# Kernel optimization log

Measured on AMD Instinct MI355X. Metric: run time of the kernel, lower is better.

The kernel has to match this reference:

```python
import jax, jax.numpy as jnp
import numpy as np

B, N, DIM, H, HD = 8, 1024, 512, 8, 64
INNER = H * HD  # 512
KS = 5


def setup_inputs() -> dict:
    key = jax.random.key(0)
    ks = jax.random.split(key, 9)
    r = lambda k, shape, s=1.0: jax.random.normal(k, shape, dtype=jnp.float32) * s
    return {
        "x_1": r(ks[0], (B, N, DIM)),
        "x_2": r(ks[1], (B, N, DIM)),
        "Wqkv1": r(ks[2], (DIM, 4 * INNER), 0.02),
        "Wqkv2": r(ks[3], (DIM, 4 * INNER), 0.02),
        "Wout1": r(ks[4], (INNER, DIM), 0.02),
        "bout1": jnp.zeros((DIM,), jnp.float32),
        "Wout2": r(ks[5], (INNER, DIM), 0.02),
        "bout2": jnp.zeros((DIM,), jnp.float32),
        "conv_w": r(ks[6], (N, 1, KS), 0.1),   # depthwise Conv1d weight [out=N, in/groups=1, k]
        "conv_b": r(ks[7], (N,), 0.02),
    }


def _split_heads(t):
    # 'b n (h d) -> b h n d'
    b, n, _ = t.shape
    return t.reshape(b, n, H, HD).transpose(0, 2, 1, 3)


def _merge_heads(t):
    # 'b h n d -> b n (h d)'
    b, h, n, d = t.shape
    return t.transpose(0, 2, 1, 3).reshape(b, n, h * d)


def reference(x_1, x_2, Wqkv1, Wqkv2, Wout1, bout1, Wout2, bout2, conv_w, conv_b):
    scale = HD ** (-0.5)
    q1, k1, v1, s1 = map(_split_heads, jnp.split(x_1 @ Wqkv1, 4, axis=-1))
    q2, k2, v2, s2 = map(_split_heads, jnp.split(x_2 @ Wqkv2, 4, axis=-1))

    dots1 = jnp.einsum('bhid,bhjd->bhij', q1, k1) * scale
    dots2 = jnp.einsum('bhid,bhjd->bhij', q2, k2) * scale

    MS = _merge_heads(s1 + s2)  # [b, n, inner_dim]
    # depthwise conv over the feature axis, channels = tokens (n), kernel 5 pad 2
    A = jax.lax.conv_general_dilated(
        MS, conv_w, window_strides=(1,), padding=((KS // 2, KS // 2),),
        dimension_numbers=('NCH', 'OIH', 'NCH'), feature_group_count=N,
    ) + conv_b[None, :, None]
    MSg = jax.nn.sigmoid(A) * MS
    MSh = _split_heads(MSg)
    dots3 = jnp.einsum('bhid,bhjd->bhij', MSh, MSh) * scale

    a1 = jax.nn.softmax(dots1, axis=-1)
    a2 = jax.nn.softmax(dots2, axis=-1)
    a3 = jax.nn.softmax(dots3, axis=-1)

    t1 = jnp.einsum('bhij,bhjd->bhid', a3, v1) + v1
    t1 = jnp.einsum('bhij,bhjd->bhid', a1, t1)
    t2 = jnp.einsum('bhij,bhjd->bhid', a3, v2) + v2
    t2 = jnp.einsum('bhij,bhjd->bhid', a2, t2)

    out1 = _merge_heads(t1) @ Wout1 + bout1
    out2 = _merge_heads(t2) @ Wout2 + bout2
    return (out1, out2)
```

## Files before the change

### kernel.cpp

```cpp
#include <hip/hip_runtime.h>
#include <hip/hip_bf16.h>

#define B_     8
#define N_     1024
#define DIM_   512
#define H_     8
#define HD_    64
#define INNER_ 512
#define QKVC   2048
#define M_     8192

typedef __attribute__((ext_vector_type(8))) short short8;
typedef __attribute__((ext_vector_type(4))) float f32x4;
#define MFMA_BF16 __builtin_amdgcn_mfma_f32_16x16x32_bf16

__device__ __forceinline__ unsigned short f2b(float x) {
    __hip_bfloat16 h = __float2bfloat16(x);
    unsigned short u; __builtin_memcpy(&u, &h, 2); return u;
}
__device__ __forceinline__ unsigned int packsplit(float x) {
    unsigned int hb = f2b(x);
    float fh = __uint_as_float(hb << 16);
    unsigned int lb = f2b(x - fh);
    return (hb << 16) | lb;
}
__device__ __forceinline__ void split8(const float* v, short8& h, short8& l) {
#pragma unroll
    for (int i = 0; i < 8; i++) {
        unsigned int hb = f2b(v[i]);
        float fh = __uint_as_float(hb << 16);
        h[i] = (short)hb; l[i] = (short)f2b(v[i] - fh);
    }
}
__device__ __forceinline__ void split2x2(float a, float b, unsigned int& h, unsigned int& l) {
    unsigned int ha = f2b(a), hb = f2b(b);
    float fa = __uint_as_float(ha << 16), fb = __uint_as_float(hb << 16);
    h = ha | (hb << 16);
    l = (unsigned int)f2b(a - fa) | ((unsigned int)f2b(b - fb) << 16);
}

__device__ __forceinline__ void gll16(const unsigned short* g, unsigned short* l) {
    __builtin_amdgcn_global_load_lds(
        (const __attribute__((address_space(1))) void*)g,
        (__attribute__((address_space(3))) void*)l, 16, 0, 0);
}


__global__ __launch_bounds__(256)
void pack_a_tiled(const float* __restrict__ in, unsigned short* __restrict__ out)
{
    size_t i = ((size_t)blockIdx.x * 256 + threadIdx.x) * 4;
    float4 v = *(const float4*)(in + i);
    const size_t R = i >> 9;
    const int k  = (int)(i & 511);
    const int kt = k >> 5, kk = k & 31;
    const int r  = (int)(R & 127);
    const size_t rt = R >> 7;
    unsigned short* tile = out + (((rt << 4) + kt) << 13) + r * 64;
    unsigned int h01, l01, h23, l23;
    split2x2(v.x, v.y, h01, l01);
    split2x2(v.z, v.w, h23, l23);
    uint2 hv; hv.x = h01; hv.y = h23;
    uint2 lv; lv.x = l01; lv.y = l23;
    const int s7 = r & 7;
    *(uint2*)&tile[(((kk >> 3)     ^ s7) << 3) + (kk & 7)] = hv;
    *(uint2*)&tile[((((kk >> 3)+4) ^ s7) << 3) + (kk & 7)] = lv;
}

__global__ __launch_bounds__(256)
void pack_w_tiled(const float* __restrict__ W, unsigned short* __restrict__ out, int N)
{
    const int n  = blockIdx.x * 256 + threadIdx.x;
    const int k0 = blockIdx.y * 4;
    float f0 = W[(size_t)(k0 + 0) * N + n];
    float f1 = W[(size_t)(k0 + 1) * N + n];
    float f2 = W[(size_t)(k0 + 2) * N + n];
    float f3 = W[(size_t)(k0 + 3) * N + n];
    const int r  = n & 127;
    const size_t rt = n >> 7;
    const int kt = k0 >> 5, kk = k0 & 31;
    unsigned short* tile = out + (((rt << 4) + kt) << 13) + r * 64;
    unsigned int h01, l01, h23, l23;
    split2x2(f0, f1, h01, l01);
    split2x2(f2, f3, h23, l23);
    uint2 hv; hv.x = h01; hv.y = h23;
    uint2 lv; lv.x = l01; lv.y = l23;
    const int s7 = r & 7;
    *(uint2*)&tile[(((kk >> 3)     ^ s7) << 3) + (kk & 7)] = hv;
    *(uint2*)&tile[((((kk >> 3)+4) ^ s7) << 3) + (kk & 7)] = lv;
}

__global__ __launch_bounds__(256)
void pack_wt(const float* __restrict__ W, unsigned int* __restrict__ Wt, int N)
{
    const int n = blockIdx.x * 256 + threadIdx.x;
    const int k0 = blockIdx.y * 4;
    uint4 p;
    p.x = packsplit(W[(size_t)(k0 + 0) * N + n]);
    p.y = packsplit(W[(size_t)(k0 + 1) * N + n]);
    p.z = packsplit(W[(size_t)(k0 + 2) * N + n]);
    p.w = packsplit(W[(size_t)(k0 + 3) * N + n]);
    *(uint4*)&Wt[(size_t)n * 512 + k0] = p;
}

template<bool BIAS, bool PACKK>
__global__ __launch_bounds__(256)
void gemm_gll(const unsigned short* __restrict__ At, const unsigned short* __restrict__ Bt,
              const float* __restrict__ bias, float* __restrict__ Cp,
              int M, int N)
{
    __shared__ __align__(16) unsigned short sA[128 * 64];
    __shared__ __align__(16) unsigned short sB[128 * 64];

    const int t    = threadIdx.x;
    const int lane = t & 63;
    const int w    = t >> 6;
    const int n16  = lane & 15, quad = lane >> 4;
    const int wm   = w >> 1, wn = w & 1;
    const int m0 = blockIdx.y * 128, n0 = blockIdx.x * 128;

    f32x4 acc[4][4];
#pragma unroll
    for (int mt = 0; mt < 4; mt++)
#pragma unroll
        for (int nt = 0; nt < 4; nt++) acc[mt][nt] = (f32x4){0.f, 0.f, 0.f, 0.f};

    const unsigned short* Ag = At + ((size_t)blockIdx.y << 4) * 8192 + (w * 64 + lane) * 8;
    const unsigned short* Bg = Bt + ((size_t)blockIdx.x << 4) * 8192 + (w * 64 + lane) * 8;
    unsigned short* sAw = &sA[w * 512];
    unsigned short* sBw = &sB[w * 512];

    for (int kt = 0; kt < 16; kt++) {
        __syncthreads();
        const size_t ko = (size_t)kt * 8192;
#pragma unroll
        for (int i = 0; i < 4; i++) {
            gll16(Ag + ko + i * 2048, sAw + i * 2048);
            gll16(Bg + ko + i * 2048, sBw + i * 2048);
        }
        __syncthreads();

        short8 Ah[4], Al[4];
#pragma unroll
        for (int mt = 0; mt < 4; mt++) {
            const int row = 64 * wm + 16 * mt + n16;
            const int base = row * 64;
            const int s7 = row & 7;
            Ah[mt] = *(const short8*)&sA[base + (((quad    ) ^ s7) << 3)];
            Al[mt] = *(const short8*)&sA[base + (((quad + 4) ^ s7) << 3)];
        }
#pragma unroll
        for (int nt = 0; nt < 4; nt++) {
            const int row = 64 * wn + 16 * nt + n16;
            const int base = row * 64;
            const int s7 = row & 7;
            short8 Bh = *(const short8*)&sB[base + (((quad    ) ^ s7) << 3)];
            short8 Bl = *(const short8*)&sB[base + (((quad + 4) ^ s7) << 3)];
#pragma unroll
            for (int mt = 0; mt < 4; mt++) {
                acc[mt][nt] = MFMA_BF16(Ah[mt], Bh, acc[mt][nt], 0, 0, 0);
                acc[mt][nt] = MFMA_BF16(Al[mt], Bh, acc[mt][nt], 0, 0, 0);
                acc[mt][nt] = MFMA_BF16(Ah[mt], Bl, acc[mt][nt], 0, 0, 0);
            }
        }
    }

    const bool packout = PACKK && ((n0 >> 9) == 1);
    float bv[4];
#pragma unroll
    for (int nt = 0; nt < 4; nt++)
        bv[nt] = BIAS ? bias[n0 + 64 * wn + 16 * nt + n16] : 0.f;
#pragma unroll
    for (int mt = 0; mt < 4; mt++) {
        const int rbase = m0 + 64 * wm + 16 * mt + 4 * quad;
#pragma unroll
        for (int r = 0; r < 4; r++) {
#pragma unroll
            for (int nt = 0; nt < 4; nt++) {
                const int col = n0 + 64 * wn + 16 * nt + n16;
                const int row = rbase + r;
                const float v = acc[mt][nt][r] + bv[nt];
                if (packout) {
                    const int dg = col & 511;
                    unsigned int hb = f2b(v);
                    float fh = __uint_as_float(hb << 16);
                    unsigned short* kim = (unsigned short*)Cp + (size_t)row * (2 * N);
                    kim[1024 + dg] = (unsigned short)hb;
                    kim[1536 + dg] = f2b(v - fh);
                } else {
                    Cp[(size_t)row * N + col] = v;
                }
            }
        }
    }
}

template<bool BIAS>
__global__ __launch_bounds__(256)
void gemm_mfma(const unsigned int* __restrict__ Ap, const unsigned int* __restrict__ Btp,
               const float* __restrict__ bias, float* __restrict__ Cp,
               int M, int N)
{
    const int K = 512;
    __shared__ __align__(16) unsigned short sA[128 * 64];
    __shared__ __align__(16) unsigned short sB[128 * 64];

    const int t    = threadIdx.x;
    const int lane = t & 63;
    const int w    = t >> 6;
    const int n16  = lane & 15, quad = lane >> 4;
    const int wm   = w >> 1, wn = w & 1;
    const int m0 = blockIdx.y * 128, n0 = blockIdx.x * 128;

    f32x4 acc[4][4];
#pragma unroll
    for (int mt = 0; mt < 4; mt++)
#pragma unroll
        for (int nt = 0; nt < 4; nt++) acc[mt][nt] = (f32x4){0.f, 0.f, 0.f, 0.f};

    const int srow = t >> 1;
    const int kb   = (t & 1) * 16;
    const unsigned int* ag = Ap  + (size_t)(m0 + srow) * K + kb;
    const unsigned int* bg = Btp + (size_t)(n0 + srow) * K + kb;
    const int s7s = srow & 7;
    unsigned short* swA = &sA[srow * 64];
    unsigned short* swB = &sB[srow * 64];

    for (int k0 = 0; k0 < K; k0 += 32) {
        __syncthreads();
#pragma unroll
        for (int i = 0; i < 4; i++) {
            const int kk = kb + i * 4;
            const int ch = kk >> 3;
            const int ho = kk & 4;
            const int c_hi = ((ch    ) ^ s7s) << 3;
            const int c_lo = ((ch + 4) ^ s7s) << 3;
            uint4 va = *(const uint4*)(ag + k0 + i * 4);
            uint4 vb = *(const uint4*)(bg + k0 + i * 4);
            uint2 ha, la, hb, lb;
            ha.x = (va.y & 0xFFFF0000u) | (va.x >> 16);
            ha.y = (va.w & 0xFFFF0000u) | (va.z >> 16);
            la.x = (va.y << 16) | (va.x & 0xFFFFu);
            la.y = (va.w << 16) | (va.z & 0xFFFFu);
            hb.x = (vb.y & 0xFFFF0000u) | (vb.x >> 16);
            hb.y = (vb.w & 0xFFFF0000u) | (vb.z >> 16);
            lb.x = (vb.y << 16) | (vb.x & 0xFFFFu);
            lb.y = (vb.w << 16) | (vb.z & 0xFFFFu);
            *(uint2*)&swA[c_hi + ho] = ha;
            *(uint2*)&swA[c_lo + ho] = la;
            *(uint2*)&swB[c_hi + ho] = hb;
            *(uint2*)&swB[c_lo + ho] = lb;
        }
        __syncthreads();

        short8 Ah[4], Al[4];
#pragma unroll
        for (int mt = 0; mt < 4; mt++) {
            const int row = 64 * wm + 16 * mt + n16;
            const int base = row * 64;
            const int s7 = row & 7;
            Ah[mt] = *(const short8*)&sA[base + (((quad    ) ^ s7) << 3)];
            Al[mt] = *(const short8*)&sA[base + (((quad + 4) ^ s7) << 3)];
        }
#pragma unroll
        for (int nt = 0; nt < 4; nt++) {
            const int row = 64 * wn + 16 * nt + n16;
            const int base = row * 64;
            const int s7 = row & 7;
            short8 Bh = *(const short8*)&sB[base + (((quad    ) ^ s7) << 3)];
            short8 Bl = *(const short8*)&sB[base + (((quad + 4) ^ s7) << 3)];
#pragma unroll
            for (int mt = 0; mt < 4; mt++) {
                acc[mt][nt] = MFMA_BF16(Ah[mt], Bh, acc[mt][nt], 0, 0, 0);
                acc[mt][nt] = MFMA_BF16(Al[mt], Bh, acc[mt][nt], 0, 0, 0);
                acc[mt][nt] = MFMA_BF16(Ah[mt], Bl, acc[mt][nt], 0, 0, 0);
            }
        }
    }

    float bv[4];
#pragma unroll
    for (int nt = 0; nt < 4; nt++)
        bv[nt] = BIAS ? bias[n0 + 64 * wn + 16 * nt + n16] : 0.f;
#pragma unroll
    for (int mt = 0; mt < 4; mt++) {
        const int rbase = m0 + 64 * wm + 16 * mt + 4 * quad;
#pragma unroll
        for (int r = 0; r < 4; r++) {
#pragma unroll
            for (int nt = 0; nt < 4; nt++) {
                const int col = n0 + 64 * wn + 16 * nt + n16;
                Cp[(size_t)(rbase + r) * N + col] = acc[mt][nt][r] + bv[nt];
            }
        }
    }
}

__global__ __launch_bounds__(128)
void convgate_kernel(const float* __restrict__ qkv1, const float* __restrict__ qkv2,
                     const float* __restrict__ convw,
                     const float* __restrict__ convb,
                     float* __restrict__ MSg, unsigned short* __restrict__ Kimg)
{
    __shared__ float ms[INNER_];
    const int blk = blockIdx.x;
    const int n = blk & (N_ - 1);
    const int b = blk >> 10;
    const int t = threadIdx.x;

    const float4* q1 = (const float4*)(qkv1 + (size_t)blk * QKVC + 3 * INNER_);
    const float4* q2 = (const float4*)(qkv2 + (size_t)blk * QKVC + 3 * INNER_);
    float4 v1 = q1[t], v2 = q2[t];
    float4 s;
    s.x = v1.x + v2.x; s.y = v1.y + v2.y; s.z = v1.z + v2.z; s.w = v1.w + v2.w;
    *(float4*)&ms[t * 4] = s;
    __syncthreads();

    float w[5];
#pragma unroll
    for (int k = 0; k < 5; k++) w[k] = convw[n * 5 + k];
    const float cb = convb[n];

    float out[4];
#pragma unroll
    for (int ff = 0; ff < 4; ff++) {
        int f = t * 4 + ff;
        float A = cb;
#pragma unroll
        for (int k = 0; k < 5; k++) {
            int idx = f + k - 2;
            if (idx >= 0 && idx < INNER_) A += ms[idx] * w[k];
        }
        float sg = 1.f / (1.f + __expf(-A));
        out[ff] = ms[f] * sg;
    }
    *(float4*)&MSg[(size_t)blk * INNER_ + t * 4] = make_float4(out[0], out[1], out[2], out[3]);

    const int h  = t >> 4;
    const int d0 = (4 * t) & 63;
    unsigned short hs[4], ls[4];
#pragma unroll
    for (int e = 0; e < 4; e++) {
        unsigned int hb = f2b(out[e]);
        float fh = __uint_as_float(hb << 16);
        hs[e] = (unsigned short)hb;
        ls[e] = f2b(out[e] - fh);
    }
    unsigned short* kim = Kimg + ((size_t)(b * 8 + h) * 1024 + n) * 128 + d0;
    uint2 hv; hv.x = (unsigned int)hs[0] | ((unsigned int)hs[1] << 16);
              hv.y = (unsigned int)hs[2] | ((unsigned int)hs[3] << 16);
    uint2 lv; lv.x = (unsigned int)ls[0] | ((unsigned int)ls[1] << 16);
              lv.y = (unsigned int)ls[2] | ((unsigned int)ls[3] << 16);
    *(uint2*)kim        = hv;
    *(uint2*)(kim + 64) = lv;
}

template<int NV, bool RESID, bool PACKO, bool IMGO, bool VIMG, int NPROB>
__global__ __launch_bounds__(512, 2)
void mattn_kernel(const float* __restrict__ Q0, const float* __restrict__ Q1,
                  const unsigned short* __restrict__ K0, const unsigned short* __restrict__ K1,
                  const float* __restrict__ VA0, const float* __restrict__ VA1,
                  const float* __restrict__ VB0, const float* __restrict__ VB1,
                  float* __restrict__ OA0, float* __restrict__ OA1,
                  float* __restrict__ OB0, float* __restrict__ OB1,
                  long long q_sb, long long q_sh, int q_sr,
                  long long k_sb, long long k_sh, int k_rs, int k_po,
                  long long v_sb, long long v_sh, int v_sr,
                  long long o_sb, long long o_sh, int o_sr)
{
    __shared__ __align__(16) unsigned short sK[64 * 128];
    __shared__ __align__(16) unsigned short sV0[64 * 64];
    __shared__ __align__(16) unsigned short sV1[(NV == 2) ? 64 * 64 : 8];
    __shared__ __align__(16) unsigned short sP[128 * 64];

    const int t    = threadIdx.x;
    const int w    = t >> 6;
    const int lane = t & 63;
    const int n16  = lane & 15;
    const int quad = lane >> 4;

    const int bid = blockIdx.x;
    const int c   = bid & 7;
    const int r1  = bid >> 3;
    const int qt  = r1 & 7;
    const int r2  = r1 >> 3;
    const int g   = r2 & 7;
    const int p   = (NPROB == 2) ? (r2 >> 3) : 0;
    const int bh  = 8 * g + c;
    const int b = bh >> 3, h = bh & 7;
    const int i0 = qt * 128;

    const float* Qb          = (NPROB == 2 && p) ? Q1 : Q0;
    const unsigned short* Kb = (NPROB == 2 && p) ? K1 : K0;
    const float* VAb         = (NPROB == 2 && p) ? VA1 : VA0;
    float* OAb               = (NPROB == 2 && p) ? OA1 : OA0;

    const float* Qg          = Qb + (size_t)b * q_sb + (size_t)h * q_sh;
    const unsigned short* Kg = Kb + (size_t)b * k_sb + (size_t)h * k_sh;

    const float* V0g = nullptr;
    const float* V1g = nullptr;
    const unsigned short* Vus = nullptr;
    if constexpr (VIMG) {
        Vus = (const unsigned short*)VAb + (size_t)b * v_sb + (size_t)h * v_sh;
    } else {
        V0g = VAb + (size_t)b * v_sb + (size_t)h * v_sh;
        if constexpr (NV == 2)
            V1g = VB0 + (size_t)b * v_sb + (size_t)h * v_sh;
    }

    float* O0g = nullptr; float* O1g = nullptr;
    unsigned short* img0 = nullptr; unsigned short* img1 = nullptr;
    if constexpr (IMGO) {
        img0 = (unsigned short*)OAb + (size_t)b * o_sb + (size_t)h * o_sh;
        if constexpr (NV == 2)
            img1 = (unsigned short*)OB0 + (size_t)b * o_sb + (size_t)h * o_sh;
    } else {
        O0g = OAb + (size_t)b * o_sb + (size_t)h * o_sh;
        if constexpr (NV == 2)
            O1g = OB0 + (size_t)b * o_sb + (size_t)h * o_sh;
    }

    const float SC2 = 0.1803368801f;
    short8 Qh[2], Ql[2];
#pragma unroll
    for (int s = 0; s < 2; s++) {
        const float* qp = Qg + (size_t)(i0 + 16 * w + n16) * q_sr + 32 * s + 8 * quad;
        float qv[8];
        float4 q0 = *(const float4*)qp;
        float4 q1 = *(const float4*)(qp + 4);
        qv[0]=q0.x*SC2; qv[1]=q0.y*SC2; qv[2]=q0.z*SC2; qv[3]=q0.w*SC2;
        qv[4]=q1.x*SC2; qv[5]=q1.y*SC2; qv[6]=q1.z*SC2; qv[7]=q1.w*SC2;
        split8(qv, Qh[s], Ql[s]);
    }

    float m_ = -1e30f, l_ = 0.f;
    f32x4 O0a[4], O1a[(NV == 2) ? 4 : 1];
#pragma unroll
    for (int nt = 0; nt < 4; nt++) O0a[nt] = (f32x4){0.f,0.f,0.f,0.f};
    if constexpr (NV == 2) {
#pragma unroll
        for (int nt = 0; nt < 4; nt++) O1a[nt] = (f32x4){0.f,0.f,0.f,0.f};
    }

    const int prow = 16 * w + n16;
    const int vc = t & 15, vp = t >> 4;

    const int jr_l = (w << 2) + (lane >> 4);
    const int lq   = (lane & 15) ^ (jr_l & 15);
    const unsigned short* kg_base = Kg + (size_t)jr_l * k_rs
                                  + (lq >> 3) * k_po + (lq & 7) * 8;
    unsigned short* sKw = &sK[w * 512];

    for (int j0 = 0; j0 < N_; j0 += 64) {
        __syncthreads();

        {
            const unsigned short* kg = kg_base + (size_t)j0 * k_rs;
            gll16(kg, sKw);
            gll16(kg + (size_t)32 * k_rs, sKw + 4096);
        }
        if constexpr (VIMG) {
            gll16(Vus + (size_t)(j0 >> 6) * 4096 + t * 8, &sV0[w * 512]);
        } else {
            const int j = 2 * vp;
            const float* a0 = V0g + (size_t)(j0 + j) * v_sr + 4 * vc;
            float4 va = *(const float4*)a0;
            float4 vb = *(const float4*)(a0 + v_sr);
#pragma unroll
            for (int e = 0; e < 4; e++) {
                float fa = (e==0)?va.x:(e==1)?va.y:(e==2)?va.z:va.w;
                float fb = (e==0)?vb.x:(e==1)?vb.y:(e==2)?vb.z:vb.w;
                unsigned int u = (unsigned int)f2b(fa) | ((unsigned int)f2b(fb) << 16);
                const int d = 4 * vc + e;
                const int phys = (vp >> 2) ^ ((d ^ (d >> 2)) & 7);
                *(unsigned int*)&sV0[d * 64 + (phys << 3) + (j & 7)] = u;
            }
            if constexpr (NV == 2) {
                const float* a1 = V1g + (size_t)(j0 + j) * v_sr + 4 * vc;
                float4 wa = *(const float4*)a1;
                float4 wb = *(const float4*)(a1 + v_sr);
#pragma unroll
                for (int e = 0; e < 4; e++) {
                    float fa = (e==0)?wa.x:(e==1)?wa.y:(e==2)?wa.z:wa.w;
                    float fb = (e==0)?wb.x:(e==1)?wb.y:(e==2)?wb.z:wb.w;
                    unsigned int u = (unsigned int)f2b(fa) | ((unsigned int)f2b(fb) << 16);
                    const int d = 4 * vc + e;
                    const int phys = (vp >> 2) ^ ((d ^ (d >> 2)) & 7);
                    *(unsigned int*)&sV1[d * 64 + (phys << 3) + (j & 7)] = u;
                }
            }
        }
        __syncthreads();

        f32x4 accS[4];
#pragma unroll
        for (int mt = 0; mt < 4; mt++) accS[mt] = (f32x4){0.f,0.f,0.f,0.f};
#pragma unroll
        for (int s = 0; s < 2; s++) {
#pragma unroll
            for (int mt = 0; mt < 4; mt++) {
                const unsigned short* kb2 = &sK[(16 * mt + n16) * 128];
                short8 kh = *(const short8*)&kb2[(((4*s + quad)    ) ^ n16) << 3];
                short8 kl = *(const short8*)&kb2[(((4*s + quad) + 8) ^ n16) << 3];
                accS[mt] = MFMA_BF16(kl, Qh[s], accS[mt], 0, 0, 0);
                accS[mt] = MFMA_BF16(kh, Ql[s], accS[mt], 0, 0, 0);
                accS[mt] = MFMA_BF16(kh, Qh[s], accS[mt], 0, 0, 0);
            }
        }

        float tmax = -1e30f;
#pragma unroll
        for (int mt = 0; mt < 4; mt++)
#pragma unroll
            for (int r = 0; r < 4; r++) tmax = fmaxf(tmax, accS[mt][r]);
        tmax = fmaxf(tmax, __shfl_xor(tmax, 16));
        tmax = fmaxf(tmax, __shfl_xor(tmax, 32));
        if (!__all(tmax <= m_ + 11.0f)) {
            const float mnew = fmaxf(m_, tmax);
            const float alpha = __builtin_amdgcn_exp2f(m_ - mnew);
            m_ = mnew;
            l_ *= alpha;
            float ar[4];
#pragma unroll
            for (int r = 0; r < 4; r++) ar[r] = __shfl(alpha, (quad << 2) + r);
#pragma unroll
            for (int nt = 0; nt < 4; nt++) {
#pragma unroll
                for (int r = 0; r < 4; r++) O0a[nt][r] *= ar[r];
                if constexpr (NV == 2)
#pragma unroll
                    for (int r = 0; r < 4; r++) O1a[nt][r] *= ar[r];
            }
        }
        float rsum = 0.f;
#pragma unroll
        for (int mt = 0; mt < 4; mt++) {
            float p0 = __builtin_amdgcn_exp2f(accS[mt][0] - m_);
            float p1 = __builtin_amdgcn_exp2f(accS[mt][1] - m_);
            float p2 = __builtin_amdgcn_exp2f(accS[mt][2] - m_);
            float p3 = __builtin_amdgcn_exp2f(accS[mt][3] - m_);
            rsum += (p0 + p1) + (p2 + p3);
            uint2 u;
            u.x = (unsigned int)f2b(p0) | ((unsigned int)f2b(p1) << 16);
            u.y = (unsigned int)f2b(p2) | ((unsigned int)f2b(p3) << 16);
            const int phys = (2 * mt + (quad >> 1)) ^ (n16 & 7);
            *(uint2*)&sP[prow * 64 + (phys << 3) + 4 * (quad & 1)] = u;
        }
        rsum += __shfl_xor(rsum, 16);
        rsum += __shfl_xor(rsum, 32);
        l_ += rsum;

#pragma unroll
        for (int s = 0; s < 2; s++) {
            short8 Pf = *(const short8*)&sP[prow * 64 + (((4*s + quad) ^ (n16 & 7)) << 3)];
#pragma unroll
            for (int nt = 0; nt < 4; nt++) {
                const int d = 16 * nt + n16;
                const int phys = (4*s + quad) ^ ((d ^ (d >> 2)) & 7);
                short8 vf = *(const short8*)&sV0[d * 64 + (phys << 3)];
                O0a[nt] = MFMA_BF16(Pf, vf, O0a[nt], 0, 0, 0);
                if constexpr (NV == 2) {
                    short8 vf1 = *(const short8*)&sV1[d * 64 + (phys << 3)];
                    O1a[nt] = MFMA_BF16(Pf, vf1, O1a[nt], 0, 0, 0);
                }
            }
        }
    }

    float linv[4];
#pragma unroll
    for (int r = 0; r < 4; r++) linv[r] = 1.0f / __shfl(l_, (quad << 2) + r);

    if constexpr (IMGO) {
        __syncthreads();
#pragma unroll
        for (int r = 0; r < 4; r++) {
            const int row = i0 + 16 * w + 4 * quad + r;
            const int jj = (16 * w + 4 * quad + r) & 63;
            const int jg = jj >> 3, j7 = jj & 7;
#pragma unroll
            for (int nt = 0; nt < 4; nt++) {
                const int d = 16 * nt + n16;
                const int swd = (d ^ (d >> 2)) & 7;
                float v = O0a[nt][r] * linv[r];
                if constexpr (RESID) v += V0g[(size_t)row * v_sr + d];
                sP[(w >> 2) * 4096 + d * 64 + ((jg ^ swd) << 3) + j7] = f2b(v);
            }
        }
        __syncthreads();
        {
            unsigned short* dst = img0 + (size_t)qt * 8192 + t * 16;
            *(uint4*)dst       = *(const uint4*)&sP[t * 16];
            *(uint4*)(dst + 8) = *(const uint4*)&sP[t * 16 + 8];
        }
        if constexpr (NV == 2) {
            __syncthreads();
#pragma unroll
            for (int r = 0; r < 4; r++) {
                const int row = i0 + 16 * w + 4 * quad + r;
                const int jj = (16 * w + 4 * quad + r) & 63;
                const int jg = jj >> 3, j7 = jj & 7;
#pragma unroll
                for (int nt = 0; nt < 4; nt++) {
                    const int d = 16 * nt + n16;
                    const int swd = (d ^ (d >> 2)) & 7;
                    float v = O1a[nt][r] * linv[r];
                    if constexpr (RESID) v += V1g[(size_t)row * v_sr + d];
                    sP[(w >> 2) * 4096 + d * 64 + ((jg ^ swd) << 3) + j7] = f2b(v);
                }
            }
            __syncthreads();
            unsigned short* dst = img1 + (size_t)qt * 8192 + t * 16;
            *(uint4*)dst       = *(const uint4*)&sP[t * 16];
            *(uint4*)(dst + 8) = *(const uint4*)&sP[t * 16 + 8];
        }
    } else {
#pragma unroll
        for (int r = 0; r < 4; r++) {
            const int row = i0 + 16 * w + 4 * quad + r;
#pragma unroll
            for (int nt = 0; nt < 4; nt++) {
                const int col = 16 * nt + n16;
                float v = O0a[nt][r] * linv[r];
                if constexpr (PACKO)
                    ((unsigned int*)O0g)[(size_t)row * o_sr + col] = packsplit(v);
                else
                    O0g[(size_t)row * o_sr + col] = v;
                if constexpr (NV == 2) {
                    float v1 = O1a[nt][r] * linv[r];
                    if constexpr (PACKO)
                        ((unsigned int*)O1g)[(size_t)row * o_sr + col] = packsplit(v1);
                    else
                        O1g[(size_t)row * o_sr + col] = v1;
                }
            }
        }
    }
}

extern "C" void kernel_launch(void* const* d_in, const int* in_sizes, int n_in,
                              void* d_out, int out_size, void* d_ws, size_t ws_size,
                              hipStream_t stream)
{
    const float* x1    = (const float*)d_in[0];
    const float* x2    = (const float*)d_in[1];
    const float* Wqkv1 = (const float*)d_in[2];
    const float* Wqkv2 = (const float*)d_in[3];
    const float* Wout1 = (const float*)d_in[4];
    const float* bout1 = (const float*)d_in[5];
    const float* Wout2 = (const float*)d_in[6];
    const float* bout2 = (const float*)d_in[7];
    const float* convw = (const float*)d_in[8];
    const float* convb = (const float*)d_in[9];

    const size_t QKV_ELEMS = (size_t)M_ * QKVC;
    const size_t BND_ELEMS = (size_t)M_ * INNER_;
    if (ws_size < (2 * QKV_ELEMS + 5 * BND_ELEMS) * sizeof(float)) return;

    float* ws   = (float*)d_ws;
    float* qkv1 = ws;
    float* qkv2 = qkv1 + QKV_ELEMS;
    float* MSg  = qkv2 + QKV_ELEMS;
    float* u1   = MSg + BND_ELEMS;
    float* u2   = u1 + BND_ELEMS;
    float* t1m  = u2 + BND_ELEMS;
    float* t2m  = t1m + BND_ELEMS;

    unsigned short* x1t   = (unsigned short*)t1m;
    unsigned short* x2t   = (unsigned short*)t2m;
    unsigned short* KimgA = (unsigned short*)t1m;
    unsigned short* w1t   = (unsigned short*)u2;
    unsigned short* w2t   = w1t + (size_t)QKVC * DIM_ * 2;
    unsigned short* u1img = (unsigned short*)u1;
    unsigned short* u2img = (unsigned short*)u2;
    unsigned int*   wo1pt = (unsigned int*)u1;
    unsigned int*   wo2pt = wo1pt + (size_t)DIM_ * DIM_;

    dim3 blk(256);

    pack_a_tiled<<<dim3(M_ * DIM_ / 1024), blk, 0, stream>>>(x1, x1t);
    pack_a_tiled<<<dim3(M_ * DIM_ / 1024), blk, 0, stream>>>(x2, x2t);
    pack_w_tiled<<<dim3(QKVC / 256, DIM_ / 4), blk, 0, stream>>>(Wqkv1, w1t, QKVC);
    pack_w_tiled<<<dim3(QKVC / 256, DIM_ / 4), blk, 0, stream>>>(Wqkv2, w2t, QKVC);

    gemm_gll<false, true><<<dim3(QKVC / 128, M_ / 128), blk, 0, stream>>>(
        x1t, w1t, nullptr, qkv1, M_, QKVC);
    gemm_gll<false, true><<<dim3(QKVC / 128, M_ / 128), blk, 0, stream>>>(
        x2t, w2t, nullptr, qkv2, M_, QKVC);

    convgate_kernel<<<dim3(M_), dim3(128), 0, stream>>>(qkv1, qkv2, convw, convb,
                                                        MSg, KimgA);

    const long long msg_sb = (long long)N_ * INNER_, msg_sh = HD_;
    const int       msg_sr = INNER_;
    const long long qkv_sb = (long long)N_ * QKVC, qkv_sh = HD_;
    const int       qkv_sr = QKVC;
    const long long kA_sb = (long long)8 * N_ * 128, kA_sh = (long long)N_ * 128;
    const long long kB_sb = (long long)N_ * QKVC * 2;
    const long long vi_sb = (long long)H_ * N_ * HD_, vi_sh = (long long)N_ * HD_;

    mattn_kernel<2, true, false, true, false, 1><<<dim3(512), dim3(512), 0, stream>>>(
        MSg, nullptr, KimgA, nullptr,
        qkv1 + 2 * INNER_, nullptr, qkv2 + 2 * INNER_, nullptr,
        (float*)u1img, nullptr, (float*)u2img, nullptr,
        msg_sb, msg_sh, msg_sr,
        kA_sb, kA_sh, 128, 64,
        qkv_sb, qkv_sh, qkv_sr,
        vi_sb, vi_sh, HD_);

    mattn_kernel<1, false, true, false, true, 2><<<dim3(1024), dim3(512), 0, stream>>>(
        qkv1, qkv2,
        (const unsigned short*)qkv1 + 1024, (const unsigned short*)qkv2 + 1024,
        (const float*)u1img, (const float*)u2img, nullptr, nullptr,
        t1m, t2m, nullptr, nullptr,
        qkv_sb, qkv_sh, qkv_sr,
        kB_sb, 64, QKVC * 2, 512,
        vi_sb, vi_sh, HD_,
        msg_sb, msg_sh, msg_sr);

    pack_wt<<<dim3(DIM_ / 256, DIM_ / 4), blk, 0, stream>>>(Wout1, wo1pt, DIM_);
    pack_wt<<<dim3(DIM_ / 256, DIM_ / 4), blk, 0, stream>>>(Wout2, wo2pt, DIM_);

    float* out1 = (float*)d_out;
    float* out2 = out1 + (size_t)M_ * DIM_;
    gemm_mfma<true><<<dim3(DIM_ / 128, M_ / 128), blk, 0, stream>>>(
        (const unsigned int*)t1m, wo1pt, bout1, out1, M_, DIM_);
    gemm_mfma<true><<<dim3(DIM_ / 128, M_ / 128), blk, 0, stream>>>(
        (const unsigned int*)t2m, wo2pt, bout2, out2, M_, DIM_);
}
```

Measured before the change: 479.0 us.

## Double-buffer K/V tiles in attention loop and stage packed GEMM output through LDS

```diff
diff --git a/kernel.cpp b/kernel.cpp
--- a/kernel.cpp
+++ b/kernel.cpp
@@ -166,29 +166,54 @@
     }
 
     const bool packout = PACKK && ((n0 >> 9) == 1);
-    float bv[4];
-#pragma unroll
-    for (int nt = 0; nt < 4; nt++)
-        bv[nt] = BIAS ? bias[n0 + 64 * wn + 16 * nt + n16] : 0.f;
-#pragma unroll
-    for (int mt = 0; mt < 4; mt++) {
-        const int rbase = m0 + 64 * wm + 16 * mt + 4 * quad;
-#pragma unroll
-        for (int r = 0; r < 4; r++) {
-#pragma unroll
-            for (int nt = 0; nt < 4; nt++) {
-                const int col = n0 + 64 * wn + 16 * nt + n16;
-                const int row = rbase + r;
-                const float v = acc[mt][nt][r] + bv[nt];
-                if (packout) {
-                    const int dg = col & 511;
-                    unsigned int hb = f2b(v);
-                    float fh = __uint_as_float(hb << 16);
-                    unsigned short* kim = (unsigned short*)Cp + (size_t)row * (2 * N);
-                    kim[1024 + dg] = (unsigned short)hb;
-                    kim[1536 + dg] = f2b(v - fh);
-                } else {
-                    Cp[(size_t)row * N + col] = v;
+    if (packout) {
+        const int col0 = n0 - 512;
+#pragma unroll 1
+        for (int pass = 0; pass < 2; pass++) {
+            __syncthreads();
+            if (wm == pass) {
+#pragma unroll
+                for (int mt = 0; mt < 4; mt++)
+#pragma unroll
+                    for (int r = 0; r < 4; r++)
+#pragma unroll
+                        for (int nt = 0; nt < 4; nt++) {
+                            const int rr = 16 * mt + 4 * quad + r;
+                            const int cl = 64 * wn + 16 * nt + n16;
+                            const float v = acc[mt][nt][r];
+                            unsigned int hb = f2b(v);
+                            float fh = __uint_as_float(hb << 16);
+                            const int off = rr * 128 + ((((cl >> 3) ^ (rr & 7)) << 3)) + (cl & 7);
+                            sA[off] = (unsigned short)hb;
+                            sB[off] = f2b(v - fh);
+                        }
+            }
+            __syncthreads();
+            const int rr = t >> 2, seg = t & 3;
+            const int row = m0 + pass * 64 + rr;
+            unsigned short* kim = (unsigned short*)Cp + (size_t)row * (2 * N)
+                                + 1024 + col0 + seg * 32;
+#pragma unroll
+            for (int i = 0; i < 4; i++) {
+                const int po = rr * 128 + ((((seg * 4 + i) ^ (rr & 7))) << 3);
+                *(uint4*)(kim + 8 * i)       = *(const uint4*)&sA[po];
+                *(uint4*)(kim + 512 + 8 * i) = *(const uint4*)&sB[po];
+            }
+        }
+    } else {
+        float bv[4];
+#pragma unroll
+        for (int nt = 0; nt < 4; nt++)
+            bv[nt] = BIAS ? bias[n0 + 64 * wn + 16 * nt + n16] : 0.f;
+#pragma unroll
+        for (int mt = 0; mt < 4; mt++) {
+            const int rbase = m0 + 64 * wm + 16 * mt + 4 * quad;
+#pragma unroll
+            for (int r = 0; r < 4; r++) {
+#pragma unroll
+                for (int nt = 0; nt < 4; nt++) {
+                    const int col = n0 + 64 * wn + 16 * nt + n16;
+                    Cp[(size_t)(rbase + r) * N + col] = acc[mt][nt][r] + bv[nt];
                 }
             }
         }
@@ -368,8 +393,8 @@
                   long long v_sb, long long v_sh, int v_sr,
                   long long o_sb, long long o_sh, int o_sr)
 {
-    __shared__ __align__(16) unsigned short sK[64 * 128];
-    __shared__ __align__(16) unsigned short sV0[64 * 64];
+    __shared__ __align__(16) unsigned short sK[2 * 64 * 128];
+    __shared__ __align__(16) unsigned short sV0[(VIMG ? 2 : 1) * 64 * 64];
     __shared__ __align__(16) unsigned short sV1[(NV == 2) ? 64 * 64 : 8];
     __shared__ __align__(16) unsigned short sP[128 * 64];
 
@@ -452,21 +477,42 @@
                                   + (lq >> 3) * k_po + (lq & 7) * 8;
     unsigned short* sKw = &sK[w * 512];
 
+    if constexpr (VIMG) {
+        gll16(kg_base, sKw);
+        gll16(kg_base + (size_t)32 * k_rs, sKw + 4096);
+        gll16(Vus + t * 8, &sV0[w * 512]);
+        const unsigned short* kg1 = kg_base + (size_t)64 * k_rs;
+        gll16(kg1, sKw + 8192);
+        gll16(kg1 + (size_t)32 * k_rs, sKw + 8192 + 4096);
+        gll16(Vus + 4096 + t * 8, &sV0[4096 + w * 512]);
+    } else {
+        gll16(kg_base, sKw);
+        gll16(kg_base + (size_t)32 * k_rs, sKw + 4096);
+    }
+    __builtin_amdgcn_sched_barrier(0);
+
+    int buf = 0;
+#pragma unroll 1
     for (int j0 = 0; j0 < N_; j0 += 64) {
-        __syncthreads();
-
-        {
-            const unsigned short* kg = kg_base + (size_t)j0 * k_rs;
-            gll16(kg, sKw);
-            gll16(kg + (size_t)32 * k_rs, sKw + 4096);
-        }
-        if constexpr (VIMG) {
-            gll16(Vus + (size_t)(j0 >> 6) * 4096 + t * 8, &sV0[w * 512]);
-        } else {
+        if constexpr (!VIMG) {
             const int j = 2 * vp;
             const float* a0 = V0g + (size_t)(j0 + j) * v_sr + 4 * vc;
             float4 va = *(const float4*)a0;
             float4 vb = *(const float4*)(a0 + v_sr);
+            float4 wa, wb;
+            if constexpr (NV == 2) {
+                const float* a1 = V1g + (size_t)(j0 + j) * v_sr + 4 * vc;
+                wa = *(const float4*)a1;
+                wb = *(const float4*)(a1 + v_sr);
+            }
+            __builtin_amdgcn_sched_barrier(0);
+            if (j0 < N_ - 64) {
+                const unsigned short* kg = kg_base + (size_t)(j0 + 64) * k_rs;
+                unsigned short* dK = &sK[(buf ^ 1) * 8192 + w * 512];
+                gll16(kg, dK);
+                gll16(kg + (size_t)32 * k_rs, dK + 4096);
+            }
+            __builtin_amdgcn_sched_barrier(0);
 #pragma unroll
             for (int e = 0; e < 4; e++) {
                 float fa = (e==0)?va.x:(e==1)?va.y:(e==2)?va.z:va.w;
@@ -477,9 +523,6 @@
                 *(unsigned int*)&sV0[d * 64 + (phys << 3) + (j & 7)] = u;
             }
             if constexpr (NV == 2) {
-                const float* a1 = V1g + (size_t)(j0 + j) * v_sr + 4 * vc;
-                float4 wa = *(const float4*)a1;
-                float4 wb = *(const float4*)(a1 + v_sr);
 #pragma unroll
                 for (int e = 0; e < 4; e++) {
                     float fa = (e==0)?wa.x:(e==1)?wa.y:(e==2)?wa.z:wa.w;
@@ -490,9 +533,18 @@
                     *(unsigned int*)&sV1[d * 64 + (phys << 3) + (j & 7)] = u;
                 }
             }
-        }
-        __syncthreads();
-
+            if (j0 < N_ - 64) asm volatile("s_waitcnt vmcnt(2) lgkmcnt(0)" ::: "memory");
+            else              asm volatile("s_waitcnt vmcnt(0) lgkmcnt(0)" ::: "memory");
+        } else {
+            if (j0 < N_ - 64) asm volatile("s_waitcnt vmcnt(3)" ::: "memory");
+            else              asm volatile("s_waitcnt vmcnt(0)" ::: "memory");
+        }
+        __builtin_amdgcn_sched_barrier(0);
+        __builtin_amdgcn_s_barrier();
+        __builtin_amdgcn_sched_barrier(0);
+
+        const unsigned short* sKb = &sK[buf * 8192];
+        const unsigned short* sVb0 = VIMG ? &sV0[buf * 4096] : &sV0[0];
         f32x4 accS[4];
 #pragma unroll
         for (int mt = 0; mt < 4; mt++) accS[mt] = (f32x4){0.f,0.f,0.f,0.f};
@@ -500,7 +552,7 @@
         for (int s = 0; s < 2; s++) {
 #pragma unroll
             for (int mt = 0; mt < 4; mt++) {
-                const unsigned short* kb2 = &sK[(16 * mt + n16) * 128];
+                const unsigned short* kb2 = &sKb[(16 * mt + n16) * 128];
                 short8 kh = *(const short8*)&kb2[(((4*s + quad)    ) ^ n16) << 3];
                 short8 kl = *(const short8*)&kb2[(((4*s + quad) + 8) ^ n16) << 3];
                 accS[mt] = MFMA_BF16(kl, Qh[s], accS[mt], 0, 0, 0);
@@ -558,7 +610,7 @@
             for (int nt = 0; nt < 4; nt++) {
                 const int d = 16 * nt + n16;
                 const int phys = (4*s + quad) ^ ((d ^ (d >> 2)) & 7);
-                short8 vf = *(const short8*)&sV0[d * 64 + (phys << 3)];
+                short8 vf = *(const short8*)&sVb0[d * 64 + (phys << 3)];
                 O0a[nt] = MFMA_BF16(Pf, vf, O0a[nt], 0, 0, 0);
                 if constexpr (NV == 2) {
                     short8 vf1 = *(const short8*)&sV1[d * 64 + (phys << 3)];
@@ -566,6 +618,21 @@
                 }
             }
         }
+
+        __builtin_amdgcn_s_barrier();
+        __builtin_amdgcn_sched_barrier(0);
+        if constexpr (VIMG) {
+            if (j0 < N_ - 128) {
+                const int jn = j0 + 128;
+                const unsigned short* kg = kg_base + (size_t)jn * k_rs;
+                unsigned short* dK = &sK[buf * 8192 + w * 512];
+                gll16(kg, dK);
+                gll16(kg + (size_t)32 * k_rs, dK + 4096);
+                gll16(Vus + (size_t)(jn >> 6) * 4096 + t * 8, &sV0[buf * 4096 + w * 512]);
+            }
+            __builtin_amdgcn_sched_barrier(0);
+        }
+        buf ^= 1;
     }
 
     float linv[4];
```

Result: slower. 531.7 us (+11.0%).

## Pre-swizzle K images at producer and merge dual-output staging through sK

Applied to the files above, without the earlier changes.

```diff
diff --git a/kernel.cpp b/kernel.cpp
--- a/kernel.cpp
+++ b/kernel.cpp
@@ -181,12 +181,14 @@
                 const int row = rbase + r;
                 const float v = acc[mt][nt][r] + bv[nt];
                 if (packout) {
-                    const int dg = col & 511;
+                    const int hh = (col >> 6) & 7, dd = col & 63, r15 = row & 15;
                     unsigned int hb = f2b(v);
                     float fh = __uint_as_float(hb << 16);
-                    unsigned short* kim = (unsigned short*)Cp + (size_t)row * (2 * N);
-                    kim[1024 + dg] = (unsigned short)hb;
-                    kim[1536 + dg] = f2b(v - fh);
+                    unsigned short lb = f2b(v - fh);
+                    unsigned short* kim = (unsigned short*)Cp
+                        + (size_t)row * (2 * N) + 1024 + hh * 128 + (dd & 7);
+                    kim[(((dd >> 3)    ) ^ r15) << 3] = (unsigned short)hb;
+                    kim[(((dd >> 3) | 8) ^ r15) << 3] = lb;
                 } else {
                     Cp[(size_t)row * N + col] = v;
                 }
@@ -338,6 +340,7 @@
 
     const int h  = t >> 4;
     const int d0 = (4 * t) & 63;
+    const int r15 = n & 15;
     unsigned short hs[4], ls[4];
 #pragma unroll
     for (int e = 0; e < 4; e++) {
@@ -346,13 +349,13 @@
         hs[e] = (unsigned short)hb;
         ls[e] = f2b(out[e] - fh);
     }
-    unsigned short* kim = Kimg + ((size_t)(b * 8 + h) * 1024 + n) * 128 + d0;
+    unsigned short* kim = Kimg + ((size_t)(b * 8 + h) * 1024 + n) * 128 + (d0 & 7);
     uint2 hv; hv.x = (unsigned int)hs[0] | ((unsigned int)hs[1] << 16);
               hv.y = (unsigned int)hs[2] | ((unsigned int)hs[3] << 16);
     uint2 lv; lv.x = (unsigned int)ls[0] | ((unsigned int)ls[1] << 16);
               lv.y = (unsigned int)ls[2] | ((unsigned int)ls[3] << 16);
-    *(uint2*)kim        = hv;
-    *(uint2*)(kim + 64) = lv;
+    *(uint2*)&kim[(((d0 >> 3)    ) ^ r15) << 3] = hv;
+    *(uint2*)&kim[(((d0 >> 3) | 8) ^ r15) << 3] = lv;
 }
 
 template<int NV, bool RESID, bool PACKO, bool IMGO, bool VIMG, int NPROB>
@@ -364,7 +367,7 @@
                   float* __restrict__ OA0, float* __restrict__ OA1,
                   float* __restrict__ OB0, float* __restrict__ OB1,
                   long long q_sb, long long q_sh, int q_sr,
-                  long long k_sb, long long k_sh, int k_rs, int k_po,
+                  long long k_sb, long long k_sh, int k_rs,
                   long long v_sb, long long v_sh, int v_sr,
                   long long o_sb, long long o_sh, int o_sr)
 {
@@ -395,8 +398,8 @@
     const float* VAb         = (NPROB == 2 && p) ? VA1 : VA0;
     float* OAb               = (NPROB == 2 && p) ? OA1 : OA0;
 
-    const float* Qg          = Qb + (size_t)b * q_sb + (size_t)h * q_sh;
-    const unsigned short* Kg = Kb + (size_t)b * k_sb + (size_t)h * k_sh;
+    const float* Qg          = Qb  + (size_t)b * q_sb + (size_t)h * q_sh;
+    const unsigned short* Kg = Kb  + (size_t)b * k_sb + (size_t)h * k_sh;
 
     const float* V0g = nullptr;
     const float* V1g = nullptr;
@@ -446,10 +449,8 @@
     const int prow = 16 * w + n16;
     const int vc = t & 15, vp = t >> 4;
 
-    const int jr_l = (w << 2) + (lane >> 4);
-    const int lq   = (lane & 15) ^ (jr_l & 15);
-    const unsigned short* kg_base = Kg + (size_t)jr_l * k_rs
-                                  + (lq >> 3) * k_po + (lq & 7) * 8;
+    const unsigned short* kg_base = Kg + (size_t)((w << 2) + (lane >> 4)) * k_rs
+                                       + ((lane & 15) << 3);
     unsigned short* sKw = &sK[w * 512];
 
     for (int j0 = 0; j0 < N_; j0 += 64) {
@@ -583,9 +584,15 @@
             for (int nt = 0; nt < 4; nt++) {
                 const int d = 16 * nt + n16;
                 const int swd = (d ^ (d >> 2)) & 7;
+                const int off = (w >> 2) * 4096 + d * 64 + ((jg ^ swd) << 3) + j7;
                 float v = O0a[nt][r] * linv[r];
                 if constexpr (RESID) v += V0g[(size_t)row * v_sr + d];
-                sP[(w >> 2) * 4096 + d * 64 + ((jg ^ swd) << 3) + j7] = f2b(v);
+                sP[off] = f2b(v);
+                if constexpr (NV == 2) {
+                    float v1 = O1a[nt][r] * linv[r];
+                    if constexpr (RESID) v1 += V1g[(size_t)row * v_sr + d];
+                    sK[off] = f2b(v1);
+                }
             }
         }
         __syncthreads();
@@ -595,25 +602,9 @@
             *(uint4*)(dst + 8) = *(const uint4*)&sP[t * 16 + 8];
         }
         if constexpr (NV == 2) {
-            __syncthreads();
-#pragma unroll
-            for (int r = 0; r < 4; r++) {
-                const int row = i0 + 16 * w + 4 * quad + r;
-                const int jj = (16 * w + 4 * quad + r) & 63;
-                const int jg = jj >> 3, j7 = jj & 7;
-#pragma unroll
-                for (int nt = 0; nt < 4; nt++) {
-                    const int d = 16 * nt + n16;
-                    const int swd = (d ^ (d >> 2)) & 7;
-                    float v = O1a[nt][r] * linv[r];
-                    if constexpr (RESID) v += V1g[(size_t)row * v_sr + d];
-                    sP[(w >> 2) * 4096 + d * 64 + ((jg ^ swd) << 3) + j7] = f2b(v);
-                }
-            }
-            __syncthreads();
             unsigned short* dst = img1 + (size_t)qt * 8192 + t * 16;
-            *(uint4*)dst       = *(const uint4*)&sP[t * 16];
-            *(uint4*)(dst + 8) = *(const uint4*)&sP[t * 16 + 8];
+            *(uint4*)dst       = *(const uint4*)&sK[t * 16];
+            *(uint4*)(dst + 8) = *(const uint4*)&sK[t * 16 + 8];
         }
     } else {
 #pragma unroll
@@ -697,7 +688,7 @@
     const long long qkv_sb = (long long)N_ * QKVC, qkv_sh = HD_;
     const int       qkv_sr = QKVC;
     const long long kA_sb = (long long)8 * N_ * 128, kA_sh = (long long)N_ * 128;
-    const long long kB_sb = (long long)N_ * QKVC * 2;
+    const long long kB_sb = (long long)N_ * QKVC * 2, kB_sh = 128;
     const long long vi_sb = (long long)H_ * N_ * HD_, vi_sh = (long long)N_ * HD_;
 
     mattn_kernel<2, true, false, true, false, 1><<<dim3(512), dim3(512), 0, stream>>>(
@@ -705,7 +696,7 @@
         qkv1 + 2 * INNER_, nullptr, qkv2 + 2 * INNER_, nullptr,
         (float*)u1img, nullptr, (float*)u2img, nullptr,
         msg_sb, msg_sh, msg_sr,
-        kA_sb, kA_sh, 128, 64,
+        kA_sb, kA_sh, 128,
         qkv_sb, qkv_sh, qkv_sr,
         vi_sb, vi_sh, HD_);
 
@@ -715,7 +706,7 @@
         (const float*)u1img, (const float*)u2img, nullptr, nullptr,
         t1m, t2m, nullptr, nullptr,
         qkv_sb, qkv_sh, qkv_sr,
-        kB_sb, 64, QKVC * 2, 512,
+        kB_sb, kB_sh, QKVC * 2,
         vi_sb, vi_sh, HD_,
         msg_sb, msg_sh, msg_sr);
 
```

New measurement: 500.1 us. 4.4% more time.
